# Optimization experiments

Measured on AMD Instinct MI355X. Metric: run time of the kernel, lower is better.

Reference implementation:

```python
import jax, jax.numpy as jnp
import numpy as np

N = 100000   # nodes
E = 250000   # edges per relation
R = 4        # relations (etypes)
H = 4        # heads
D = 32       # per-head dim = hid_size // n_heads
IN = 256
HID = 128    # H * D
OUT = 64
SLOPE = 0.2  # DGL GATConv leaky_relu negative_slope


def setup_inputs() -> dict:
    key = jax.random.key(0)
    ks = jax.random.split(key, 16)
    rn = lambda k, shp, s: jax.random.normal(k, shp, dtype=jnp.float32) * s
    return {
        "x": rn(ks[0], (N, IN), 1.0),
        "src": jax.random.randint(ks[1], (R, E), 0, N, dtype=jnp.int32),
        "dst": jax.random.randint(ks[2], (R, E), 0, N, dtype=jnp.int32),
        "W0": rn(ks[3], (R, IN, HID), IN ** -0.5),
        "al0": rn(ks[4], (R, H, D), D ** -0.5),
        "ar0": rn(ks[5], (R, H, D), D ** -0.5),
        "b0": jnp.zeros((R, HID), jnp.float32),
        "W1": rn(ks[6], (R, HID, HID), HID ** -0.5),
        "al1": rn(ks[7], (R, H, D), D ** -0.5),
        "ar1": rn(ks[8], (R, H, D), D ** -0.5),
        "b1": jnp.zeros((R, HID), jnp.float32),
        "W2": rn(ks[9], (R, HID, HID), HID ** -0.5),
        "al2": rn(ks[10], (R, H, D), D ** -0.5),
        "ar2": rn(ks[11], (R, H, D), D ** -0.5),
        "b2": jnp.zeros((R, HID), jnp.float32),
        "fcW": rn(ks[12], (HID, OUT), HID ** -0.5),
        "fcb": jnp.zeros((OUT,), jnp.float32),
    }


def hetero_gat_layer(h, src, dst, W, al, ar, b):
    """HeteroGraphConv({etype: GATConv}, aggregate='sum') for one layer.

    h: [N, F_in]; W: [R, F_in, HID]; al/ar: [R, H, D]; b: [R, HID];
    src/dst: [R, E] int edge lists per relation.  Returns [N, HID].
    """
    feat = jnp.einsum('nf,rfo->rno', h, W).reshape(R, N, H, D)
    el = jnp.einsum('rnhd,rhd->rnh', feat, al)  # [R, N, H]
    er = jnp.einsum('rnhd,rhd->rnh', feat, ar)  # [R, N, H]

    def per_rel(feat_r, el_r, er_r, s, d, b_r):
        e = jax.nn.leaky_relu(el_r[s] + er_r[d], SLOPE)  # [E, H]
        # edge softmax over incoming edges of each destination node
        emax = jax.lax.stop_gradient(jax.ops.segment_max(e, d, num_segments=N))
        ee = jnp.exp(e - emax[d])
        denom = jax.ops.segment_sum(ee, d, num_segments=N)  # [N, H]
        alpha = ee / jnp.maximum(denom[d], 1e-9)             # [E, H]
        msg = feat_r[s] * alpha[:, :, None]                  # [E, H, D]
        out = jax.ops.segment_sum(msg, d, num_segments=N)    # [N, H, D]
        return out + b_r.reshape(H, D)                       # GATConv bias

    outs = jax.vmap(per_rel)(feat, el, er, src, dst, b)      # [R, N, H, D]
    # HeteroGraphConv aggregate='sum' across relations, then flatten heads
    return outs.sum(0).reshape(N, H * D)


def reference(x, src, dst, W0, al0, ar0, b0, W1, al1, ar1, b1, W2, al2, ar2, b2, fcW, fcb):
    h = jax.nn.relu(hetero_gat_layer(x, src, dst, W0, al0, ar0, b0))  # dropout = identity (eval)
    h = jax.nn.relu(hetero_gat_layer(h, src, dst, W1, al1, ar1, b1))
    h = hetero_gat_layer(h, src, dst, W2, al2, ar2, b2)               # last layer: no relu
    return h @ fcW + fcb                                              # self.fc on predict_category
```

## Files before the change

kernel.cpp:

```cpp
#include <hip/hip_runtime.h>
#include <hip/hip_bf16.h>

#define N_NODES 100000
#define N_EDGES 250000
#define N_REL 4
#define N_HEAD 4
#define D_HEAD 32
#define F_IN 256
#define F_HID 128
#define F_OUT 64
#define LRELU_SLOPE 0.2f

#define N_TILES 782
#define N_TGRP ((N_TILES + 7) / 8)
#define GEMM_BLOCKS (N_TGRP * 40)

#define SCAN_B 256
#define NBLK ((N_NODES + SCAN_B - 1) / SCAN_B)

typedef __attribute__((ext_vector_type(8))) short s16x8;
typedef __attribute__((ext_vector_type(8))) unsigned short u16x8;
typedef __attribute__((ext_vector_type(4))) unsigned short u16x4;
typedef __attribute__((ext_vector_type(4))) float f32x4;

__device__ __forceinline__ float bf2f(unsigned short u) {
    return __uint_as_float(((unsigned int)u) << 16);
}
__device__ __forceinline__ unsigned short f2bf(float f) {
    unsigned int x = __float_as_uint(f);
    unsigned int r = x + 0x7fffu + ((x >> 16) & 1u);
    return (unsigned short)(r >> 16);
}
__device__ __forceinline__ void gload_lds16(const void* g, void* l) {
    __builtin_amdgcn_global_load_lds(
        (const __attribute__((address_space(1))) unsigned int*)g,
        (__attribute__((address_space(3))) unsigned int*)l, 16, 0, 0);
}

template<int FIN>
__global__ __launch_bounds__(256) void gemm_mfma_k(const unsigned short* __restrict__ A,
                                                   const unsigned short* __restrict__ BtAll,
                                                   const unsigned short* __restrict__ WalBt,
                                                   unsigned short* __restrict__ CAll,
                                                   float* __restrict__ el,
                                                   float* __restrict__ er) {
    const int g = blockIdx.x;
    const int grp = g / 40;
    const int rem = g - grp * 40;
    const int rel = rem >> 3;
    const int t = grp * 8 + (rem & 7);
    if (t >= N_TILES) return;
    const int row0 = t * 128;
    const unsigned short* Bt = (rel < N_REL) ? BtAll + (size_t)rel * F_HID * FIN : WalBt;

    __shared__ short As[128 * 64];
    __shared__ short Bs[128 * 64];
    const int tid = threadIdx.x;
    const int lane = tid & 63;
    const int wave = tid >> 6;
    const int wr = wave >> 1, wc = wave & 1;

    f32x4 acc[4][4];
#pragma unroll
    for (int m = 0; m < 4; ++m)
#pragma unroll
        for (int n = 0; n < 4; ++n) acc[m][n] = (f32x4)0.f;

    for (int k0 = 0; k0 < FIN; k0 += 64) {
        if (k0) __syncthreads();
#pragma unroll
        for (int i = 0; i < 4; ++i) {
            int flat = i * 256 + tid;
            int r = flat >> 3, ch = flat & 7;
            int sch = ch ^ (r & 7);
            int grow = row0 + r; if (grow > N_NODES - 1) grow = N_NODES - 1;
            gload_lds16(A + (size_t)grow * FIN + k0 + sch * 8, As + (size_t)flat * 8);
        }
#pragma unroll
        for (int i = 0; i < 4; ++i) {
            int flat = i * 256 + tid;
            int r = flat >> 3, ch = flat & 7;
            int sch = ch ^ (r & 7);
            gload_lds16(Bt + (size_t)r * FIN + k0 + sch * 8, Bs + (size_t)flat * 8);
        }
        __syncthreads();
#pragma unroll
        for (int kk = 0; kk < 2; ++kk) {
            s16x8 a[4], b[4];
            const int kb = kk * 64 + (lane >> 4) * 16;
#pragma unroll
            for (int m = 0; m < 4; ++m) {
                int r = wr * 64 + m * 16 + (lane & 15);
                int off = r * 128 + (kb ^ ((r & 7) << 4));
                a[m] = *(const s16x8*)((const char*)As + off);
            }
#pragma unroll
            for (int n = 0; n < 4; ++n) {
                int r = wc * 64 + n * 16 + (lane & 15);
                int off = r * 128 + (kb ^ ((r & 7) << 4));
                b[n] = *(const s16x8*)((const char*)Bs + off);
            }
#pragma unroll
            for (int m = 0; m < 4; ++m)
#pragma unroll
                for (int n = 0; n < 4; ++n)
                    acc[m][n] = __builtin_amdgcn_mfma_f32_16x16x32_bf16(b[n], a[m], acc[m][n], 0, 0, 0);
        }
    }
    if (rel < N_REL) {
        unsigned short* C = CAll + (size_t)rel * N_NODES * F_HID;
#pragma unroll
        for (int m = 0; m < 4; ++m) {
            int r = row0 + wr * 64 + m * 16 + (lane & 15);
            if (r < N_NODES) {
#pragma unroll
                for (int n = 0; n < 4; ++n) {
                    int cbase = wc * 64 + n * 16 + (lane >> 4) * 4;
                    u16x4 o = {f2bf(acc[m][n][0]), f2bf(acc[m][n][1]),
                               f2bf(acc[m][n][2]), f2bf(acc[m][n][3])};
                    *(u16x4*)(C + (size_t)r * F_HID + cbase) = o;
                }
            }
        }
    } else if (wc == 0) {
        int relh = lane >> 4;
#pragma unroll
        for (int m = 0; m < 4; ++m) {
            int r = row0 + wr * 64 + m * 16 + (lane & 15);
            if (r < N_NODES) {
                *(f32x4*)(el + (size_t)relh * N_NODES * N_HEAD + r * 4) = acc[m][0];
                *(f32x4*)(er + (size_t)relh * N_NODES * N_HEAD + r * 4) = acc[m][1];
            }
        }
    }
}

template<int K>
__global__ __launch_bounds__(256) void wprep2_k(const float* __restrict__ W,
                                                const float* __restrict__ al,
                                                const float* __restrict__ ar,
                                                unsigned short* __restrict__ Wt,
                                                unsigned short* __restrict__ walbt) {
    int i = blockIdx.x * 256 + threadIdx.x;
    const int nWt = N_REL * K * 128;
    if (i < nWt) {
        int r = i / (K * 128);
        int rem = i - r * K * 128;
        int k = rem >> 7, n = rem & 127;
        Wt[(size_t)r * 128 * K + (size_t)n * K + k] = f2bf(W[i]);
        return;
    }
    i -= nWt;
    const int nWal = N_REL * K * 4;
    if (i < nWal) {
        int rel = i / (K * 4);
        int rem = i - rel * K * 4;
        int f = rem >> 2, h = rem & 3;
        const float* wrow = W + ((size_t)rel * K + f) * F_HID + h * D_HEAD;
        const float* alv = al + ((size_t)rel * N_HEAD + h) * D_HEAD;
        const float* arv = ar + ((size_t)rel * N_HEAD + h) * D_HEAD;
        float sl = 0.f, sr = 0.f;
#pragma unroll
        for (int d = 0; d < D_HEAD; ++d) {
            float w = wrow[d];
            sl += w * alv[d];
            sr += w * arv[d];
        }
        walbt[(size_t)(rel * 4 + h) * K + f] = f2bf(sl);
        walbt[(size_t)(16 + rel * 4 + h) * K + f] = f2bf(sr);
        return;
    }
    i -= nWal;
    if (i < 96 * K) walbt[(size_t)32 * K + i] = 0;
}

__global__ __launch_bounds__(256) void cast_k(const float* __restrict__ in,
                                              unsigned short* __restrict__ out, int n4) {
    int i = blockIdx.x * 256 + threadIdx.x;
    if (i >= n4) return;
    float4 v = *(const float4*)(in + (size_t)i * 4);
    u16x4 o = {f2bf(v.x), f2bf(v.y), f2bf(v.z), f2bf(v.w)};
    *(u16x4*)(out + (size_t)i * 4) = o;
}

__global__ __launch_bounds__(256) void count_k(const int* __restrict__ dst, int* __restrict__ cnt) {
    int e = blockIdx.x * 256 + threadIdx.x;
    if (e >= N_EDGES) return;
    int r = blockIdx.y;
    atomicAdd(&cnt[r * N_NODES + dst[(size_t)r * N_EDGES + e]], 1);
}

__global__ __launch_bounds__(SCAN_B) void scan1_k(const int* __restrict__ cnt,
                                                  int* __restrict__ row, int* __restrict__ bsum) {
    __shared__ int sdata[SCAN_B];
    int r = blockIdx.y;
    int n = blockIdx.x * SCAN_B + threadIdx.x;
    int v = (n < N_NODES) ? cnt[r * N_NODES + n] : 0;
    sdata[threadIdx.x] = v;
    __syncthreads();
    for (int off = 1; off < SCAN_B; off <<= 1) {
        int t = (threadIdx.x >= off) ? sdata[threadIdx.x - off] : 0;
        __syncthreads();
        sdata[threadIdx.x] += t;
        __syncthreads();
    }
    if (n < N_NODES) row[r * (N_NODES + 1) + n] = sdata[threadIdx.x] - v;
    if (threadIdx.x == SCAN_B - 1) bsum[r * NBLK + blockIdx.x] = sdata[threadIdx.x];
}

__global__ __launch_bounds__(512) void scan2_k(int* __restrict__ bsum) {
    __shared__ int sdata[512];
    int r = blockIdx.x;
    int v = (threadIdx.x < NBLK) ? bsum[r * NBLK + threadIdx.x] : 0;
    sdata[threadIdx.x] = v;
    __syncthreads();
    for (int off = 1; off < 512; off <<= 1) {
        int t = (threadIdx.x >= off) ? sdata[threadIdx.x - off] : 0;
        __syncthreads();
        sdata[threadIdx.x] += t;
        __syncthreads();
    }
    if (threadIdx.x < NBLK) bsum[r * NBLK + threadIdx.x] = sdata[threadIdx.x] - v;
}

__global__ __launch_bounds__(256) void scan3_k(int* __restrict__ row, const int* __restrict__ bsum) {
    int r = blockIdx.y;
    int n = blockIdx.x * 256 + threadIdx.x;
    if (n > N_NODES) return;
    if (n == N_NODES) { row[r * (N_NODES + 1) + N_NODES] = N_EDGES; return; }
    row[r * (N_NODES + 1) + n] += bsum[r * NBLK + n / SCAN_B];
}

__global__ __launch_bounds__(256) void fill_k(const int* __restrict__ src, const int* __restrict__ dst,
                                              const int* __restrict__ row, int* __restrict__ cursor,
                                              int* __restrict__ csr_src) {
    int e = blockIdx.x * 256 + threadIdx.x;
    if (e >= N_EDGES) return;
    int r = blockIdx.y;
    int s = src[(size_t)r * N_EDGES + e];
    int d = dst[(size_t)r * N_EDGES + e];
    int p = row[r * (N_NODES + 1) + d] + atomicAdd(&cursor[r * N_NODES + d], 1);
    csr_src[(size_t)r * N_EDGES + p] = s;
}

__global__ __launch_bounds__(256) void gather_fused_k(const int* __restrict__ csr_srcAll,
                                                      const int* __restrict__ rowAll,
                                                      const unsigned short* __restrict__ featAll,
                                                      const float* __restrict__ el,
                                                      const float* __restrict__ er,
                                                      const float* __restrict__ bias,
                                                      unsigned short* __restrict__ hbf,
                                                      int relu) {
    int j = blockIdx.x * 256 + threadIdx.x;
    if (j >= N_NODES * 16) return;
    int n = j >> 4, sub = j & 15;
    int h = sub >> 2;
    float acc[8];
#pragma unroll
    for (int q = 0; q < 8; ++q) acc[q] = 0.f;

#pragma unroll
    for (int rel = 0; rel < N_REL; ++rel) {
        const int* row = rowAll + (size_t)rel * (N_NODES + 1);
        const int* cs = csr_srcAll + (size_t)rel * N_EDGES;
        const float* elr = el + (size_t)rel * N_NODES * N_HEAD;
        const unsigned short* feat = featAll + (size_t)rel * N_NODES * F_HID;
        int st = row[n], en = row[n + 1];
        if (st == en) continue;
        float erd = er[(size_t)rel * N_NODES * N_HEAD + n * 4 + h];
        float sum = 0.f;
        float racc[8];
#pragma unroll
        for (int q = 0; q < 8; ++q) racc[q] = 0.f;
        int p = st;
        for (; p + 2 <= en; p += 2) {
            int s0 = cs[p], s1 = cs[p + 1];
            float e0 = elr[s0 * 4 + h];
            float e1 = elr[s1 * 4 + h];
            u16x8 f0 = *(const u16x8*)(feat + (size_t)s0 * F_HID + sub * 8);
            u16x8 f1 = *(const u16x8*)(feat + (size_t)s1 * F_HID + sub * 8);
            float v0 = e0 + erd; v0 = v0 > 0.f ? v0 : LRELU_SLOPE * v0;
            float v1 = e1 + erd; v1 = v1 > 0.f ? v1 : LRELU_SLOPE * v1;
            float ee0 = __expf(v0), ee1 = __expf(v1);
            sum += ee0; sum += ee1;
#pragma unroll
            for (int q = 0; q < 8; ++q) {
                racc[q] += ee0 * bf2f(f0[q]);
                racc[q] += ee1 * bf2f(f1[q]);
            }
        }
        if (p < en) {
            int s = cs[p];
            float v = elr[s * 4 + h] + erd;
            v = v > 0.f ? v : LRELU_SLOPE * v;
            float ee = __expf(v);
            sum += ee;
            u16x8 f = *(const u16x8*)(feat + (size_t)s * F_HID + sub * 8);
#pragma unroll
            for (int q = 0; q < 8; ++q) racc[q] += ee * bf2f(f[q]);
        }
        float id = 1.f / fmaxf(sum, 1e-30f);
#pragma unroll
        for (int q = 0; q < 8; ++q) acc[q] += racc[q] * id;
    }

    int c0 = sub * 8;
    u16x8 o;
#pragma unroll
    for (int q = 0; q < 8; ++q) {
        int c = c0 + q;
        float bs = bias[c] + bias[128 + c] + bias[256 + c] + bias[384 + c];
        float t = acc[q] + bs;
        if (relu) t = fmaxf(t, 0.f);
        o[q] = f2bf(t);
    }
    *(u16x8*)(hbf + (size_t)n * F_HID + c0) = o;
}

__global__ __launch_bounds__(256) void fc_k(const unsigned short* __restrict__ Hm,
                                            const float* __restrict__ Wm,
                                            const float* __restrict__ bv,
                                            float* __restrict__ out) {
    __shared__ float Ws[F_HID][F_OUT];
    __shared__ float Hs[32][F_HID];
    const int tid = threadIdx.x;
    const int n0 = blockIdx.x * 32;
    const int tx = tid & 63, ty = tid >> 6;
#pragma unroll
    for (int l = 0; l < 8; ++l) {
        int flat = tid + l * 256;
        int r = flat >> 4, c4 = flat & 15;
        *(float4*)(&Ws[r][c4 * 4]) = *(const float4*)(Wm + r * F_OUT + c4 * 4);
    }
#pragma unroll
    for (int l = 0; l < 2; ++l) {
        int flat = tid + l * 256;
        int r = flat >> 4, c8 = flat & 15;
        u16x8 v = (u16x8)0;
        if (n0 + r < N_NODES)
            v = *(const u16x8*)(Hm + (size_t)(n0 + r) * F_HID + c8 * 8);
#pragma unroll
        for (int q = 0; q < 8; ++q) Hs[r][c8 * 8 + q] = bf2f(v[q]);
    }
    __syncthreads();
    float acc[8];
#pragma unroll
    for (int i = 0; i < 8; ++i) acc[i] = 0.f;
    for (int k = 0; k < F_HID; ++k) {
        float w = Ws[k][tx];
#pragma unroll
        for (int i = 0; i < 8; ++i) acc[i] += Hs[ty * 8 + i][k] * w;
    }
    float bb = bv[tx];
#pragma unroll
    for (int i = 0; i < 8; ++i) {
        int r = n0 + ty * 8 + i;
        if (r < N_NODES) out[(size_t)r * F_OUT + tx] = acc[i] + bb;
    }
}

extern "C" void kernel_launch(void* const* d_in, const int* in_sizes, int n_in,
                              void* d_out, int out_size, void* d_ws, size_t ws_size,
                              hipStream_t stream) {
    const float* x   = (const float*)d_in[0];
    const int*   src = (const int*)d_in[1];
    const int*   dst = (const int*)d_in[2];
    const float* W[3]  = {(const float*)d_in[3], (const float*)d_in[7],  (const float*)d_in[11]};
    const float* al[3] = {(const float*)d_in[4], (const float*)d_in[8],  (const float*)d_in[12]};
    const float* ar[3] = {(const float*)d_in[5], (const float*)d_in[9],  (const float*)d_in[13]};
    const float* bb[3] = {(const float*)d_in[6], (const float*)d_in[10], (const float*)d_in[14]};
    const float* fcW = (const float*)d_in[15];
    const float* fcb = (const float*)d_in[16];
    float* out = (float*)d_out;

    char* p = (char*)d_ws;
    unsigned short* hbf   = (unsigned short*)p; p += (size_t)N_NODES * F_IN * 2;
    unsigned short* featb = (unsigned short*)p; p += (size_t)N_REL * N_NODES * F_HID * 2;
    float* el    = (float*)p;               p += (size_t)N_REL * N_NODES * N_HEAD * 4;
    float* er    = (float*)p;               p += (size_t)N_REL * N_NODES * N_HEAD * 4;
    unsigned short* walbt0 = (unsigned short*)p; p += (size_t)128 * F_IN * 2;
    unsigned short* walbt1 = (unsigned short*)p; p += (size_t)128 * F_HID * 2;
    unsigned short* walbt2 = (unsigned short*)p; p += (size_t)128 * F_HID * 2;
    unsigned short* Wt0   = (unsigned short*)p; p += (size_t)N_REL * F_IN * F_HID * 2;
    unsigned short* Wt1   = (unsigned short*)p; p += (size_t)N_REL * F_HID * F_HID * 2;
    unsigned short* Wt2   = (unsigned short*)p; p += (size_t)N_REL * F_HID * F_HID * 2;
    int* cnt     = (int*)p;                 p += (size_t)N_REL * N_NODES * 4;
    int* cursor  = (int*)p;                 p += (size_t)N_REL * N_NODES * 4;
    int* rowp    = (int*)p;                 p += (size_t)N_REL * (N_NODES + 1) * 4;
    int* bsum    = (int*)p;                 p += (size_t)N_REL * NBLK * 4;
    int* csr_src = (int*)p;                 p += (size_t)N_REL * N_EDGES * 4;

    const int eblk = (N_EDGES + 255) / 256;
    const dim3 egrid(eblk, N_REL);

    cast_k<<<(N_NODES * F_IN / 4 + 255) / 256, 256, 0, stream>>>(x, hbf, N_NODES * F_IN / 4);
    wprep2_k<F_IN><<<(N_REL * F_IN * 132 + 96 * F_IN + 255) / 256, 256, 0, stream>>>(
        W[0], al[0], ar[0], Wt0, walbt0);
    wprep2_k<F_HID><<<(N_REL * F_HID * 132 + 96 * F_HID + 255) / 256, 256, 0, stream>>>(
        W[1], al[1], ar[1], Wt1, walbt1);
    wprep2_k<F_HID><<<(N_REL * F_HID * 132 + 96 * F_HID + 255) / 256, 256, 0, stream>>>(
        W[2], al[2], ar[2], Wt2, walbt2);

    hipMemsetAsync(cnt, 0, 2 * (size_t)N_REL * N_NODES * sizeof(int), stream);
    count_k<<<egrid, 256, 0, stream>>>(dst, cnt);
    scan1_k<<<dim3(NBLK, N_REL), SCAN_B, 0, stream>>>(cnt, rowp, bsum);
    scan2_k<<<N_REL, 512, 0, stream>>>(bsum);
    scan3_k<<<dim3((N_NODES + 256) / 256, N_REL), 256, 0, stream>>>(rowp, bsum);
    fill_k<<<egrid, 256, 0, stream>>>(src, dst, rowp, cursor, csr_src);

    const int g_blocks  = (N_NODES * 16 + 255) / 256;
    const int fc_blocks = (N_NODES + 31) / 32;

    const unsigned short* Wts[3] = {Wt0, Wt1, Wt2};
    const unsigned short* walbts[3] = {walbt0, walbt1, walbt2};

    for (int layer = 0; layer < 3; ++layer) {
        if (layer == 0)
            gemm_mfma_k<F_IN><<<GEMM_BLOCKS, 256, 0, stream>>>(hbf, Wts[0], walbts[0],
                                                               featb, el, er);
        else
            gemm_mfma_k<F_HID><<<GEMM_BLOCKS, 256, 0, stream>>>(hbf, Wts[layer], walbts[layer],
                                                                featb, el, er);
        gather_fused_k<<<g_blocks, 256, 0, stream>>>(csr_src, rowp, featb, el, er,
                                                     bb[layer], hbf, layer < 2 ? 1 : 0);
    }
    fc_k<<<fc_blocks, 256, 0, stream>>>(hbf, fcW, fcb, out);
}
```

Measured before the change: 513.7 us.

## Bucket nodes by total in-degree to balance gather warps

Adds a counting sort of destination nodes by summed in-degree across relations (degree, histogram, bin scan, placement kernels), giving a permutation. The fused gather kernel then processes nodes in permuted order so each wavefront handles nodes of similar degree, which is meant to reduce divergence from uneven per-node loop lengths. The cost is three small extra kernels, one of them a single-thread scan, plus an indirection load. Output writes and the neighbouring-node locality of hbf and el/er accesses become scattered, and the atomic placement order is nondeterministic.

```diff
diff --git a/kernel.cpp b/kernel.cpp
--- a/kernel.cpp
+++ b/kernel.cpp
@@ -17,6 +17,7 @@
 
 #define SCAN_B 256
 #define NBLK ((N_NODES + SCAN_B - 1) / SCAN_B)
+#define DEG_BINS 64
 
 typedef __attribute__((ext_vector_type(8))) short s16x8;
 typedef __attribute__((ext_vector_type(8))) unsigned short u16x8;
@@ -243,8 +244,39 @@
     csr_src[(size_t)r * N_EDGES + p] = s;
 }
 
+__global__ __launch_bounds__(256) void deg_k(const int* __restrict__ rowAll,
+                                             int* __restrict__ deg, int* __restrict__ hist) {
+    int n = blockIdx.x * 256 + threadIdx.x;
+    if (n >= N_NODES) return;
+    int d = 0;
+#pragma unroll
+    for (int r = 0; r < N_REL; ++r)
+        d += rowAll[r * (N_NODES + 1) + n + 1] - rowAll[r * (N_NODES + 1) + n];
+    d = d < DEG_BINS ? d : DEG_BINS - 1;
+    deg[n] = d;
+    atomicAdd(&hist[d], 1);
+}
+
+__global__ void binscan_k(const int* __restrict__ hist, int* __restrict__ base) {
+    if (threadIdx.x == 0) {
+        int acc = 0;
+        for (int i = 0; i < DEG_BINS; ++i) { base[i] = acc; acc += hist[i]; }
+    }
+}
+
+__global__ __launch_bounds__(256) void place_k(const int* __restrict__ deg,
+                                               const int* __restrict__ base,
+                                               int* __restrict__ cur, int* __restrict__ perm) {
+    int n = blockIdx.x * 256 + threadIdx.x;
+    if (n >= N_NODES) return;
+    int d = deg[n];
+    int pos = base[d] + atomicAdd(&cur[d], 1);
+    perm[pos] = n;
+}
+
 __global__ __launch_bounds__(256) void gather_fused_k(const int* __restrict__ csr_srcAll,
                                                       const int* __restrict__ rowAll,
+                                                      const int* __restrict__ perm,
                                                       const unsigned short* __restrict__ featAll,
                                                       const float* __restrict__ el,
                                                       const float* __restrict__ er,
@@ -253,7 +285,8 @@
                                                       int relu) {
     int j = blockIdx.x * 256 + threadIdx.x;
     if (j >= N_NODES * 16) return;
-    int n = j >> 4, sub = j & 15;
+    int n = perm[j >> 4];
+    int sub = j & 15;
     int h = sub >> 2;
     float acc[8];
 #pragma unroll
@@ -386,12 +419,18 @@
     unsigned short* Wt2   = (unsigned short*)p; p += (size_t)N_REL * F_HID * F_HID * 2;
     int* cnt     = (int*)p;                 p += (size_t)N_REL * N_NODES * 4;
     int* cursor  = (int*)p;                 p += (size_t)N_REL * N_NODES * 4;
+    int* hist    = (int*)p;                 p += DEG_BINS * 4;
+    int* bincur  = (int*)p;                 p += DEG_BINS * 4;
+    int* binbase = (int*)p;                 p += DEG_BINS * 4;
     int* rowp    = (int*)p;                 p += (size_t)N_REL * (N_NODES + 1) * 4;
     int* bsum    = (int*)p;                 p += (size_t)N_REL * NBLK * 4;
     int* csr_src = (int*)p;                 p += (size_t)N_REL * N_EDGES * 4;
+    int* deg     = (int*)p;                 p += (size_t)N_NODES * 4;
+    int* perm    = (int*)p;                 p += (size_t)N_NODES * 4;
 
     const int eblk = (N_EDGES + 255) / 256;
     const dim3 egrid(eblk, N_REL);
+    const int nblk256 = (N_NODES + 255) / 256;
 
     cast_k<<<(N_NODES * F_IN / 4 + 255) / 256, 256, 0, stream>>>(x, hbf, N_NODES * F_IN / 4);
     wprep2_k<F_IN><<<(N_REL * F_IN * 132 + 96 * F_IN + 255) / 256, 256, 0, stream>>>(
@@ -401,12 +440,15 @@
     wprep2_k<F_HID><<<(N_REL * F_HID * 132 + 96 * F_HID + 255) / 256, 256, 0, stream>>>(
         W[2], al[2], ar[2], Wt2, walbt2);
 
-    hipMemsetAsync(cnt, 0, 2 * (size_t)N_REL * N_NODES * sizeof(int), stream);
+    hipMemsetAsync(cnt, 0, 2 * (size_t)N_REL * N_NODES * sizeof(int) + 2 * DEG_BINS * 4, stream);
     count_k<<<egrid, 256, 0, stream>>>(dst, cnt);
     scan1_k<<<dim3(NBLK, N_REL), SCAN_B, 0, stream>>>(cnt, rowp, bsum);
     scan2_k<<<N_REL, 512, 0, stream>>>(bsum);
     scan3_k<<<dim3((N_NODES + 256) / 256, N_REL), 256, 0, stream>>>(rowp, bsum);
     fill_k<<<egrid, 256, 0, stream>>>(src, dst, rowp, cursor, csr_src);
+    deg_k<<<nblk256, 256, 0, stream>>>(rowp, deg, hist);
+    binscan_k<<<1, 64, 0, stream>>>(hist, binbase);
+    place_k<<<nblk256, 256, 0, stream>>>(deg, binbase, bincur, perm);
 
     const int g_blocks  = (N_NODES * 16 + 255) / 256;
     const int fc_blocks = (N_NODES + 31) / 32;
@@ -421,7 +463,7 @@
         else
             gemm_mfma_k<F_HID><<<GEMM_BLOCKS, 256, 0, stream>>>(hbf, Wts[layer], walbts[layer],
                                                                 featb, el, er);
-        gather_fused_k<<<g_blocks, 256, 0, stream>>>(csr_src, rowp, featb, el, er,
+        gather_fused_k<<<g_blocks, 256, 0, stream>>>(csr_src, rowp, perm, featb, el, er,
                                                      bb[layer], hbf, layer < 2 ? 1 : 0);
     }
     fc_k<<<fc_blocks, 256, 0, stream>>>(hbf, fcW, fcb, out);
```

New measurement: 1.220 ms. +137.5%, slower.
